# Kernel optimization log

Hardware: AMD Instinct MI355X
Metric: run time of the kernel (lower is better)

The kernel has to match this reference:

```python
import jax, jax.numpy as jnp
import numpy as np
import math

HIDDEN = 2048
NUM_HEADS = 16
HEAD_SIZE = HIDDEN // NUM_HEADS
BATCH = 2
SEQ = 2048


def setup_inputs() -> dict:
    key = jax.random.key(0)
    k_x, k_wq, k_bq, k_wo, k_bo = jax.random.split(key, 5)
    scale_in = 1.0 / math.sqrt(HIDDEN)
    return {
        "x": jax.random.normal(k_x, (BATCH, SEQ, HIDDEN), dtype=jnp.float32),
        # torch Linear stored as W[out,in]; we keep the jax-friendly transpose [in,out]
        "Wqkv": jax.random.normal(k_wq, (HIDDEN, 3 * HIDDEN), dtype=jnp.float32) * scale_in,
        "bqkv": jax.random.normal(k_bq, (3 * HIDDEN,), dtype=jnp.float32) * 0.01,
        "Wo": jax.random.normal(k_wo, (HIDDEN, HIDDEN), dtype=jnp.float32) * scale_in,
        "bo": jax.random.normal(k_bo, (HIDDEN,), dtype=jnp.float32) * 0.01,
    }


def reference(x, Wqkv, bqkv, Wo, bo):
    b, s, _ = x.shape
    # fused QKV projection; channel layout is (three, num_heads, head_size)
    kqv = x @ Wqkv + bqkv                      # [b, s, 3*hidden]
    kqv = kqv.reshape(b, s, 3, NUM_HEADS, HEAD_SIZE)
    q = kqv[:, :, 0]                           # [b, s, n, h]
    k = kqv[:, :, 1]
    v = kqv[:, :, 2]
    # scores[b, n, s_key, t_query] = K_s . Q_t, scaled
    scores = jnp.einsum('bsnh,btnh->bnst', k, q) / math.sqrt(HEAD_SIZE)
    # faithful to original: keep upper triangle (key <= query), masked entries are exactly -10000
    ones = jnp.ones_like(scores)
    scores = jnp.triu(scores) + (-10000.0) * jnp.tril(ones, k=-1)
    attn = jax.nn.softmax(scores, axis=2)      # softmax over key dim
    out = jnp.einsum('bnkq,bknh->bqnh', attn, v)  # [b, s, n, h]
    out = out.reshape(b, s, NUM_HEADS * HEAD_SIZE)
    return out @ Wo + bo
```

## Files before the change

kernel.cpp:

```cpp
#include <hip/hip_runtime.h>
#include <hip/hip_bf16.h>

typedef __hip_bfloat16 bf16;
typedef __attribute__((ext_vector_type(8))) short short8;
typedef __attribute__((ext_vector_type(8))) unsigned short ushort8;
typedef __attribute__((ext_vector_type(4))) float floatx4;

#define BATCH 2
#define S_LEN 2048
#define NHEAD 16
#define HD 128
#define HIDDEN 2048
#define QSCALE 0.12754435f
#define FOFF 12.0f

static __device__ __forceinline__ unsigned short f2bf(float f) {
    union { float f; unsigned int u; } c; c.f = f;
    unsigned int u = c.u;
    unsigned int rounded = u + 0x7FFF + ((u >> 16) & 1);
    return (unsigned short)(rounded >> 16);
}

static __device__ __forceinline__ short8 lds_read16(unsigned off) {
    short8 r;
    asm volatile("ds_read_b128 %0, %1" : "=v"(r) : "v"(off));
    return r;
}

__global__ __launch_bounds__(256) void cast_f32_bf16(const float* __restrict__ src,
                                                     bf16* __restrict__ dst) {
    int i = (blockIdx.x * 256 + threadIdx.x) * 8;
    float4 a = *(const float4*)&src[i];
    float4 b = *(const float4*)&src[i + 4];
    ushort8 o;
    o[0] = f2bf(a.x); o[1] = f2bf(a.y); o[2] = f2bf(a.z); o[3] = f2bf(a.w);
    o[4] = f2bf(b.x); o[5] = f2bf(b.y); o[6] = f2bf(b.z); o[7] = f2bf(b.w);
    *(ushort8*)&dst[i] = o;
}

__global__ __launch_bounds__(256) void cast_transpose(const float* __restrict__ src,
                                                      bf16* __restrict__ dst,
                                                      int R, int C) {
    __shared__ unsigned short t[32][33];
    int tx = threadIdx.x & 31, ty = threadIdx.x >> 5;
    int c0 = blockIdx.x * 32, r0 = blockIdx.y * 32;
#pragma unroll
    for (int i = 0; i < 4; i++) {
        int r = r0 + ty + i * 8;
        t[ty + i * 8][tx] = f2bf(src[(size_t)r * C + c0 + tx]);
    }
    __syncthreads();
#pragma unroll
    for (int i = 0; i < 4; i++) {
        int cc = c0 + ty + i * 8;
        ((unsigned short*)dst)[(size_t)cc * R + r0 + tx] = t[tx][ty + i * 8];
    }
}

#define GK 2048
#define NT 32

#define BAR __builtin_amdgcn_s_barrier()
#define SCHED0 __builtin_amdgcn_sched_barrier(0)

static __device__ __forceinline__ void gll(const bf16* g, char* l) {
    __builtin_amdgcn_global_load_lds(
        (const __attribute__((address_space(1))) void*)g,
        (__attribute__((address_space(3))) void*)l, 16, 0, 0);
}

#define STG8(s)                                                                 \
    do {                                                                        \
        _Pragma("unroll")                                                       \
        for (int ld = 0; ld < 4; ld++) {                                        \
            gll(pA + (size_t)(ld * 8) * GK + (s) * 64,                          \
                lA + ((s) & 1) * 16384 + wave * 4096 + ld * 1024);              \
            gll(pB + (size_t)(ld * 8) * GK + (s) * 64,                          \
                lB + ((s) & 1) * 16384 + wave * 4096 + ld * 1024);              \
        }                                                                       \
    } while (0)

#define RD_A(i, ks) aF[i][ks] = lds_read16(Ab + ((unsigned)((wm * 64 + (i) * 16 + lr) << 7)) + ((unsigned)(((ks) * 64 + quad * 16)) ^ axor));
#define RD_B(j, ks) bF[j][ks] = lds_read16(Bb + ((unsigned)((wn * 64 + (j) * 16 + lr) << 7)) + ((unsigned)(((ks) * 64 + quad * 16)) ^ axor));

template <int EPI>
__global__ __launch_bounds__(256, 2) void gemm128(const bf16* __restrict__ A,
                                                  const bf16* __restrict__ Bt,
                                                  const float* __restrict__ bias,
                                                  bf16* __restrict__ Qb,
                                                  bf16* __restrict__ Kb,
                                                  bf16* __restrict__ Vt,
                                                  float* __restrict__ Cout,
                                                  int ntN) {
    __shared__ __align__(16) bf16 Asm[2][128 * 64];
    __shared__ __align__(16) bf16 Bsm[2][128 * 64];

    int tid = threadIdx.x;
    int wave = tid >> 6, lane = tid & 63;
    int quad = lane >> 4, lr = lane & 15;
    int wm = wave >> 1, wn = wave & 1;
    unsigned axor = (unsigned)((lr & 7) << 4);

    int nwg = gridDim.x;
    int cpx = nwg >> 3;
    int bid = blockIdx.x;
    int swz = (bid & 7) * cpx + (bid >> 3);
    int mt = swz / ntN, nt = swz - mt * ntN;
    int m0 = mt * 128, n0 = nt * 128;

    int srow = wave * 32 + (lane >> 3);
    int scol = ((lane & 7) ^ ((lane >> 3) & 7)) * 8;
    const bf16* pA = A + (size_t)(m0 + srow) * GK + scol;
    const bf16* pB = Bt + (size_t)(n0 + srow) * GK + scol;
    char* lA = (char*)&Asm[0][0];
    char* lB = (char*)&Bsm[0][0];

    unsigned aBase0 = (unsigned)(size_t)(__attribute__((address_space(3))) char*)lA;
    unsigned bBase0 = (unsigned)(size_t)(__attribute__((address_space(3))) char*)lB;

    const floatx4 fzero = {0.f, 0.f, 0.f, 0.f};
    floatx4 acc[4][4];
#pragma unroll
    for (int i = 0; i < 4; i++)
#pragma unroll
        for (int j = 0; j < 4; j++) acc[i][j] = fzero;

    short8 aF[4][2], bF[4][2];

    STG8(0);
    STG8(1);
    asm volatile("s_waitcnt vmcnt(8)" ::: "memory");
    BAR;

    for (int t = 0; t < NT; ++t) {
        unsigned Ab = aBase0 + (unsigned)((t & 1) * 16384);
        unsigned Bb = bBase0 + (unsigned)((t & 1) * 16384);

        RD_B(0, 0) RD_B(0, 1) RD_B(1, 0) RD_B(1, 1)
        RD_A(0, 0) RD_A(0, 1) RD_A(1, 0) RD_A(1, 1)
        RD_A(2, 0) RD_A(2, 1) RD_A(3, 0) RD_A(3, 1)
        RD_B(2, 0) RD_B(2, 1) RD_B(3, 0) RD_B(3, 1)

        asm volatile("s_waitcnt lgkmcnt(4)" ::: "memory");
        SCHED0;
        __builtin_amdgcn_s_setprio(1);
#pragma unroll
        for (int ks = 0; ks < 2; ks++)
#pragma unroll
            for (int i = 0; i < 4; i++)
#pragma unroll
                for (int j = 0; j < 2; j++)
                    acc[i][j] = __builtin_amdgcn_mfma_f32_16x16x32_bf16(
                        aF[i][ks], bF[j][ks], acc[i][j], 0, 0, 0);
        __builtin_amdgcn_s_setprio(0);

        asm volatile("s_waitcnt lgkmcnt(0)" ::: "memory");
        SCHED0;
        __builtin_amdgcn_s_setprio(1);
#pragma unroll
        for (int ks = 0; ks < 2; ks++)
#pragma unroll
            for (int i = 0; i < 4; i++)
#pragma unroll
                for (int j = 2; j < 4; j++)
                    acc[i][j] = __builtin_amdgcn_mfma_f32_16x16x32_bf16(
                        aF[i][ks], bF[j][ks], acc[i][j], 0, 0, 0);
        __builtin_amdgcn_s_setprio(0);

        BAR;
        SCHED0;
        if (t + 2 < NT) {
            STG8(t + 2);
            SCHED0;
            asm volatile("s_waitcnt vmcnt(8)" ::: "memory");
        } else {
            asm volatile("s_waitcnt vmcnt(0)" ::: "memory");
        }
        BAR;
    }

    if (EPI == 0) {
#pragma unroll
        for (int i = 0; i < 4; i++) {
#pragma unroll
            for (int j = 0; j < 4; j++) {
                int gcn = n0 + wn * 64 + j * 16 + lr;
                float bv = bias[gcn];
                int tsel = gcn >> 11, hh = (gcn >> 7) & 15, d = gcn & 127;
#pragma unroll
                for (int reg = 0; reg < 4; reg++) {
                    int gm = m0 + wm * 64 + i * 16 + quad * 4 + reg;
                    float v = acc[i][j][reg] + bv;
                    int bb = gm >> 11, s = gm & 2047;
                    size_t hb = (size_t)(bb * NHEAD + hh);
                    if (tsel == 0) {
                        Qb[(hb * S_LEN + s) * HD + d] = __float2bfloat16(v * QSCALE);
                    } else if (tsel == 1) {
                        Kb[(hb * S_LEN + s) * HD + d] = __float2bfloat16(v);
                    } else {
                        Vt[(hb * HD + d) * S_LEN + s] = __float2bfloat16(v);
                    }
                }
            }
        }
    } else {
        int N = ntN << 7;
#pragma unroll
        for (int i = 0; i < 4; i++) {
#pragma unroll
            for (int j = 0; j < 4; j++) {
                int gcn = n0 + wn * 64 + j * 16 + lr;
                float bv = bias[gcn];
#pragma unroll
                for (int reg = 0; reg < 4; reg++) {
                    int gm = m0 + wm * 64 + i * 16 + quad * 4 + reg;
                    Cout[(size_t)gm * N + gcn] = acc[i][j][reg] + bv;
                }
            }
        }
    }
}

#define PSTR 72
__global__ __launch_bounds__(256, 2) void attn_kernel(const bf16* __restrict__ Qb,
                                                      const bf16* __restrict__ Kb,
                                                      const bf16* __restrict__ Vt,
                                                      bf16* __restrict__ Obuf) {
    __shared__ __align__(16) bf16 Ks[64 * 128];
    __shared__ __align__(16) bf16 Vs[128 * 64];
    __shared__ __align__(16) bf16 Ps[4][16 * PSTR];

    int tid = threadIdx.x;
    int wave = tid >> 6, lane = tid & 63;
    int quad = lane >> 4, lr = lane & 15;
    int srow = lane >> 4;
    int head = blockIdx.x, p = blockIdx.y, b = blockIdx.z;
    size_t hb = (size_t)(b * NHEAD + head);
    const bf16* Qbase = Qb + hb * S_LEN * HD;
    const bf16* Kbase = Kb + hb * S_LEN * HD;
    const bf16* Vbase = Vt + hb * (size_t)HD * S_LEN;

    const floatx4 fzero = {0.f, 0.f, 0.f, 0.f};
    const float MASKV = -30000.f;
    short8 ones;
#pragma unroll
    for (int i = 0; i < 8; i++) ones[i] = (short)0x3F80;

    for (int sub = 0; sub < 2; sub++) {
        int qt = sub ? (31 - p) : p;
        int q0 = qt * 64;
        int niter = qt + 1;

        short8 qF[4];
#pragma unroll
        for (int kc = 0; kc < 4; kc++)
            qF[kc] = *(const short8*)&Qbase[(size_t)(q0 + wave * 16 + lr) * HD + kc * 32 + quad * 8];

        floatx4 Oacc[8];
        floatx4 lacc = fzero;
#pragma unroll
        for (int dn = 0; dn < 8; dn++) Oacc[dn] = fzero;

        ushort8 kpre[4], vpre[4];
#pragma unroll
        for (int i = 0; i < 4; i++) {
            int rl = wave * 16 + i * 4 + srow;
            int gc = lr ^ (rl & 15);
            kpre[i] = *(const ushort8*)&Kbase[(size_t)rl * HD + gc * 8];
            int vr = wave * 32 + i * 8 + (lane >> 3);
            int gvc = (lane & 7) ^ (vr & 7);
            vpre[i] = *(const ushort8*)&Vbase[(size_t)vr * S_LEN + gvc * 8];
        }

        for (int kt = 0; kt < niter; kt++) {
            __syncthreads();
#pragma unroll
            for (int i = 0; i < 4; i++) {
                *(ushort8*)&Ks[(wave * 16 + i * 4) * 128 + lane * 8] = kpre[i];
                *(ushort8*)&Vs[(wave * 32 + i * 8) * 64 + lane * 8] = vpre[i];
            }
            __syncthreads();
            if (kt + 1 < niter) {
                int ns0 = (kt + 1) * 64;
#pragma unroll
                for (int i = 0; i < 4; i++) {
                    int rl = wave * 16 + i * 4 + srow;
                    int gc = lr ^ (rl & 15);
                    kpre[i] = *(const ushort8*)&Kbase[(size_t)(ns0 + rl) * HD + gc * 8];
                    int vr = wave * 32 + i * 8 + (lane >> 3);
                    int gvc = (lane & 7) ^ (vr & 7);
                    vpre[i] = *(const ushort8*)&Vbase[(size_t)vr * S_LEN + ns0 + gvc * 8];
                }
            }

            floatx4 sc[4];
#pragma unroll
            for (int nt = 0; nt < 4; nt++) sc[nt] = fzero;
#pragma unroll
            for (int kc = 0; kc < 4; kc++)
#pragma unroll
                for (int nt = 0; nt < 4; nt++) {
                    short8 kf = *(const short8*)&Ks[(nt * 16 + lr) * 128 + (((kc * 4 + quad) ^ lr) & 15) * 8];
                    sc[nt] = __builtin_amdgcn_mfma_f32_16x16x32_bf16(qF[kc], kf, sc[nt], 0, 0, 0);
                }
            if (kt == niter - 1) {
#pragma unroll
                for (int nt = 0; nt < 4; nt++)
#pragma unroll
                    for (int reg = 0; reg < 4; reg++) {
                        int qg = wave * 16 + quad * 4 + reg;
                        int kg = nt * 16 + lr;
                        if (kg > qg) sc[nt][reg] = MASKV;
                    }
            }
#pragma unroll
            for (int nt = 0; nt < 4; nt++)
#pragma unroll
                for (int reg = 0; reg < 4; reg++) {
                    float pv = __builtin_amdgcn_exp2f(sc[nt][reg] - FOFF);
                    Ps[wave][(quad * 4 + reg) * PSTR + nt * 16 + lr] = __float2bfloat16(pv);
                }
#pragma unroll
            for (int st = 0; st < 2; st++) {
                short8 aP = *(const short8*)&Ps[wave][lr * PSTR + st * 32 + quad * 8];
                lacc = __builtin_amdgcn_mfma_f32_16x16x32_bf16(aP, ones, lacc, 0, 0, 0);
#pragma unroll
                for (int dn = 0; dn < 8; dn++) {
                    short8 vf = *(const short8*)&Vs[(dn * 16 + lr) * 64 + (((st * 4 + quad) ^ (lr & 7)) & 7) * 8];
                    Oacc[dn] = __builtin_amdgcn_mfma_f32_16x16x32_bf16(aP, vf, Oacc[dn], 0, 0, 0);
                }
            }
        }

#pragma unroll
        for (int reg = 0; reg < 4; reg++) {
            float inv = 1.0f / lacc[reg];
            int qg = q0 + wave * 16 + quad * 4 + reg;
#pragma unroll
            for (int dn = 0; dn < 8; dn++) {
                int d = dn * 16 + lr;
                Obuf[((size_t)(b * S_LEN + qg)) * HIDDEN + head * HD + d] =
                    __float2bfloat16(Oacc[dn][reg] * inv);
            }
        }
    }
}

extern "C" void kernel_launch(void* const* d_in, const int* in_sizes, int n_in,
                              void* d_out, int out_size, void* d_ws, size_t ws_size,
                              hipStream_t stream) {
    (void)in_sizes; (void)n_in; (void)out_size; (void)ws_size;
    const float* x    = (const float*)d_in[0];
    const float* Wqkv = (const float*)d_in[1];
    const float* bqkv = (const float*)d_in[2];
    const float* Wo   = (const float*)d_in[3];
    const float* bo   = (const float*)d_in[4];
    float* out = (float*)d_out;

    bf16* ws = (bf16*)d_ws;
    bf16* Xb    = ws;
    bf16* Obuf  = ws;
    bf16* WqkvT = ws + (size_t)8388608;
    bf16* WoT   = WqkvT;
    bf16* Qb    = WqkvT + (size_t)12582912;
    bf16* Kb    = Qb + (size_t)8388608;
    bf16* Vt    = Kb + (size_t)8388608;

    cast_f32_bf16<<<4096, 256, 0, stream>>>(x, Xb);
    cast_transpose<<<dim3(192, 64), 256, 0, stream>>>(Wqkv, WqkvT, 2048, 6144);
    gemm128<0><<<dim3(1536), dim3(256), 0, stream>>>(Xb, WqkvT, bqkv, Qb, Kb, Vt, nullptr, 48);
    cast_transpose<<<dim3(64, 64), 256, 0, stream>>>(Wo, WoT, 2048, 2048);
    attn_kernel<<<dim3(16, 16, 2), 256, 0, stream>>>(Qb, Kb, Vt, Obuf);
    gemm128<1><<<dim3(512), dim3(256), 0, stream>>>(Obuf, WoT, bo, nullptr, nullptr, nullptr, out, 16);
}
```

Before: 371.8 us.

## Process 128 queries per attention block to reuse K/V tiles

Each attention block now owns one 128-query tile, split into two 64-row subtiles per wave, instead of a balanced pair of 64-query tiles. Every K/V tile staged into LDS feeds both query subtiles, which halves global K/V loads and barriers per query. Causal masking is applied on the last two key tiles, and the first subtile skips the fully masked final tile. Blocks are issued heaviest first to soften the uneven per-block work. In exchange, accumulator registers double, which risks spills or lower occupancy under the launch bound of 2.

```diff
diff --git a/kernel.cpp b/kernel.cpp
--- a/kernel.cpp
+++ b/kernel.cpp
@@ -228,13 +228,14 @@
                                                       bf16* __restrict__ Obuf) {
     __shared__ __align__(16) bf16 Ks[64 * 128];
     __shared__ __align__(16) bf16 Vs[128 * 64];
-    __shared__ __align__(16) bf16 Ps[4][16 * PSTR];
+    __shared__ __align__(16) bf16 Ps[4][32 * PSTR];
 
     int tid = threadIdx.x;
     int wave = tid >> 6, lane = tid & 63;
     int quad = lane >> 4, lr = lane & 15;
     int srow = lane >> 4;
-    int head = blockIdx.x, p = blockIdx.y, b = blockIdx.z;
+    int head = blockIdx.x, b = blockIdx.z;
+    int qt = 15 - blockIdx.y;
     size_t hb = (size_t)(b * NHEAD + head);
     const bf16* Qbase = Qb + hb * S_LEN * HD;
     const bf16* Kbase = Kb + hb * S_LEN * HD;
@@ -246,102 +247,129 @@
 #pragma unroll
     for (int i = 0; i < 8; i++) ones[i] = (short)0x3F80;
 
-    for (int sub = 0; sub < 2; sub++) {
-        int qt = sub ? (31 - p) : p;
-        int q0 = qt * 64;
-        int niter = qt + 1;
-
-        short8 qF[4];
+    int q0 = qt * 128;
+    int niter = 2 * qt + 2;
+
+    short8 qF[2][4];
+#pragma unroll
+    for (int s = 0; s < 2; s++)
 #pragma unroll
         for (int kc = 0; kc < 4; kc++)
-            qF[kc] = *(const short8*)&Qbase[(size_t)(q0 + wave * 16 + lr) * HD + kc * 32 + quad * 8];
-
-        floatx4 Oacc[8];
-        floatx4 lacc = fzero;
-#pragma unroll
-        for (int dn = 0; dn < 8; dn++) Oacc[dn] = fzero;
-
-        ushort8 kpre[4], vpre[4];
+            qF[s][kc] = *(const short8*)&Qbase[(size_t)(q0 + s * 64 + wave * 16 + lr) * HD + kc * 32 + quad * 8];
+
+    floatx4 Oacc0[8], Oacc1[8];
+    floatx4 lacc0 = fzero, lacc1 = fzero;
+#pragma unroll
+    for (int dn = 0; dn < 8; dn++) { Oacc0[dn] = fzero; Oacc1[dn] = fzero; }
+
+    ushort8 kpre[4], vpre[4];
+#pragma unroll
+    for (int i = 0; i < 4; i++) {
+        int rl = wave * 16 + i * 4 + srow;
+        int gc = lr ^ (rl & 15);
+        kpre[i] = *(const ushort8*)&Kbase[(size_t)rl * HD + gc * 8];
+        int vr = wave * 32 + i * 8 + (lane >> 3);
+        int gvc = (lane & 7) ^ (vr & 7);
+        vpre[i] = *(const ushort8*)&Vbase[(size_t)vr * S_LEN + gvc * 8];
+    }
+
+    for (int kt = 0; kt < niter; kt++) {
+        __syncthreads();
 #pragma unroll
         for (int i = 0; i < 4; i++) {
-            int rl = wave * 16 + i * 4 + srow;
-            int gc = lr ^ (rl & 15);
-            kpre[i] = *(const ushort8*)&Kbase[(size_t)rl * HD + gc * 8];
-            int vr = wave * 32 + i * 8 + (lane >> 3);
-            int gvc = (lane & 7) ^ (vr & 7);
-            vpre[i] = *(const ushort8*)&Vbase[(size_t)vr * S_LEN + gvc * 8];
-        }
-
-        for (int kt = 0; kt < niter; kt++) {
-            __syncthreads();
+            *(ushort8*)&Ks[(wave * 16 + i * 4) * 128 + lane * 8] = kpre[i];
+            *(ushort8*)&Vs[(wave * 32 + i * 8) * 64 + lane * 8] = vpre[i];
+        }
+        __syncthreads();
+        if (kt + 1 < niter) {
+            int ns0 = (kt + 1) * 64;
 #pragma unroll
             for (int i = 0; i < 4; i++) {
-                *(ushort8*)&Ks[(wave * 16 + i * 4) * 128 + lane * 8] = kpre[i];
-                *(ushort8*)&Vs[(wave * 32 + i * 8) * 64 + lane * 8] = vpre[i];
-            }
-            __syncthreads();
-            if (kt + 1 < niter) {
-                int ns0 = (kt + 1) * 64;
-#pragma unroll
-                for (int i = 0; i < 4; i++) {
-                    int rl = wave * 16 + i * 4 + srow;
-                    int gc = lr ^ (rl & 15);
-                    kpre[i] = *(const ushort8*)&Kbase[(size_t)(ns0 + rl) * HD + gc * 8];
-                    int vr = wave * 32 + i * 8 + (lane >> 3);
-                    int gvc = (lane & 7) ^ (vr & 7);
-                    vpre[i] = *(const ushort8*)&Vbase[(size_t)vr * S_LEN + ns0 + gvc * 8];
+                int rl = wave * 16 + i * 4 + srow;
+                int gc = lr ^ (rl & 15);
+                kpre[i] = *(const ushort8*)&Kbase[(size_t)(ns0 + rl) * HD + gc * 8];
+                int vr = wave * 32 + i * 8 + (lane >> 3);
+                int gvc = (lane & 7) ^ (vr & 7);
+                vpre[i] = *(const ushort8*)&Vbase[(size_t)vr * S_LEN + ns0 + gvc * 8];
+            }
+        }
+
+        bool last = (kt == niter - 1);
+        bool penult = (kt == niter - 2);
+
+        floatx4 sc0[4], sc1[4];
+#pragma unroll
+        for (int nt = 0; nt < 4; nt++) { sc0[nt] = fzero; sc1[nt] = fzero; }
+#pragma unroll
+        for (int kc = 0; kc < 4; kc++)
+#pragma unroll
+            for (int nt = 0; nt < 4; nt++) {
+                short8 kf = *(const short8*)&Ks[(nt * 16 + lr) * 128 + (((kc * 4 + quad) ^ lr) & 15) * 8];
+                if (!last) sc0[nt] = __builtin_amdgcn_mfma_f32_16x16x32_bf16(qF[0][kc], kf, sc0[nt], 0, 0, 0);
+                sc1[nt] = __builtin_amdgcn_mfma_f32_16x16x32_bf16(qF[1][kc], kf, sc1[nt], 0, 0, 0);
+            }
+        if (penult) {
+#pragma unroll
+            for (int nt = 0; nt < 4; nt++)
+#pragma unroll
+                for (int reg = 0; reg < 4; reg++) {
+                    int qg = wave * 16 + quad * 4 + reg;
+                    int kg = nt * 16 + lr;
+                    if (kg > qg) sc0[nt][reg] = MASKV;
                 }
-            }
-
-            floatx4 sc[4];
-#pragma unroll
-            for (int nt = 0; nt < 4; nt++) sc[nt] = fzero;
-#pragma unroll
-            for (int kc = 0; kc < 4; kc++)
-#pragma unroll
-                for (int nt = 0; nt < 4; nt++) {
-                    short8 kf = *(const short8*)&Ks[(nt * 16 + lr) * 128 + (((kc * 4 + quad) ^ lr) & 15) * 8];
-                    sc[nt] = __builtin_amdgcn_mfma_f32_16x16x32_bf16(qF[kc], kf, sc[nt], 0, 0, 0);
+        }
+        if (last) {
+#pragma unroll
+            for (int nt = 0; nt < 4; nt++)
+#pragma unroll
+                for (int reg = 0; reg < 4; reg++) {
+                    int qg = wave * 16 + quad * 4 + reg;
+                    int kg = nt * 16 + lr;
+                    if (kg > qg) sc1[nt][reg] = MASKV;
                 }
-            if (kt == niter - 1) {
-#pragma unroll
-                for (int nt = 0; nt < 4; nt++)
-#pragma unroll
-                    for (int reg = 0; reg < 4; reg++) {
-                        int qg = wave * 16 + quad * 4 + reg;
-                        int kg = nt * 16 + lr;
-                        if (kg > qg) sc[nt][reg] = MASKV;
-                    }
-            }
-#pragma unroll
-            for (int nt = 0; nt < 4; nt++)
-#pragma unroll
-                for (int reg = 0; reg < 4; reg++) {
-                    float pv = __builtin_amdgcn_exp2f(sc[nt][reg] - FOFF);
-                    Ps[wave][(quad * 4 + reg) * PSTR + nt * 16 + lr] = __float2bfloat16(pv);
+        }
+#pragma unroll
+        for (int nt = 0; nt < 4; nt++)
+#pragma unroll
+            for (int reg = 0; reg < 4; reg++) {
+                if (!last) {
+                    float pv0 = __builtin_amdgcn_exp2f(sc0[nt][reg] - FOFF);
+                    Ps[wave][(quad * 4 + reg) * PSTR + nt * 16 + lr] = __float2bfloat16(pv0);
                 }
-#pragma unroll
-            for (int st = 0; st < 2; st++) {
-                short8 aP = *(const short8*)&Ps[wave][lr * PSTR + st * 32 + quad * 8];
-                lacc = __builtin_amdgcn_mfma_f32_16x16x32_bf16(aP, ones, lacc, 0, 0, 0);
-#pragma unroll
-                for (int dn = 0; dn < 8; dn++) {
-                    short8 vf = *(const short8*)&Vs[(dn * 16 + lr) * 64 + (((st * 4 + quad) ^ (lr & 7)) & 7) * 8];
-                    Oacc[dn] = __builtin_amdgcn_mfma_f32_16x16x32_bf16(aP, vf, Oacc[dn], 0, 0, 0);
-                }
-            }
-        }
-
-#pragma unroll
-        for (int reg = 0; reg < 4; reg++) {
-            float inv = 1.0f / lacc[reg];
-            int qg = q0 + wave * 16 + quad * 4 + reg;
+                float pv1 = __builtin_amdgcn_exp2f(sc1[nt][reg] - FOFF);
+                Ps[wave][(16 + quad * 4 + reg) * PSTR + nt * 16 + lr] = __float2bfloat16(pv1);
+            }
+#pragma unroll
+        for (int st = 0; st < 2; st++) {
+            short8 aP0;
+            if (!last) {
+                aP0 = *(const short8*)&Ps[wave][lr * PSTR + st * 32 + quad * 8];
+                lacc0 = __builtin_amdgcn_mfma_f32_16x16x32_bf16(aP0, ones, lacc0, 0, 0, 0);
+            }
+            short8 aP1 = *(const short8*)&Ps[wave][(16 + lr) * PSTR + st * 32 + quad * 8];
+            lacc1 = __builtin_amdgcn_mfma_f32_16x16x32_bf16(aP1, ones, lacc1, 0, 0, 0);
 #pragma unroll
             for (int dn = 0; dn < 8; dn++) {
-                int d = dn * 16 + lr;
-                Obuf[((size_t)(b * S_LEN + qg)) * HIDDEN + head * HD + d] =
-                    __float2bfloat16(Oacc[dn][reg] * inv);
-            }
+                short8 vf = *(const short8*)&Vs[(dn * 16 + lr) * 64 + (((st * 4 + quad) ^ (lr & 7)) & 7) * 8];
+                if (!last) Oacc0[dn] = __builtin_amdgcn_mfma_f32_16x16x32_bf16(aP0, vf, Oacc0[dn], 0, 0, 0);
+                Oacc1[dn] = __builtin_amdgcn_mfma_f32_16x16x32_bf16(aP1, vf, Oacc1[dn], 0, 0, 0);
+            }
+        }
+    }
+
+#pragma unroll
+    for (int reg = 0; reg < 4; reg++) {
+        float inv0 = 1.0f / lacc0[reg];
+        float inv1 = 1.0f / lacc1[reg];
+        int qg0 = q0 + wave * 16 + quad * 4 + reg;
+        int qg1 = qg0 + 64;
+#pragma unroll
+        for (int dn = 0; dn < 8; dn++) {
+            int d = dn * 16 + lr;
+            Obuf[((size_t)(b * S_LEN + qg0)) * HIDDEN + head * HD + d] =
+                __float2bfloat16(Oacc0[dn][reg] * inv0);
+            Obuf[((size_t)(b * S_LEN + qg1)) * HIDDEN + head * HD + d] =
+                __float2bfloat16(Oacc1[dn][reg] * inv1);
         }
     }
 }
```

Result: slower. 489.4 us (+31.6%).
